# Kernel optimization log

Measured on AMD Instinct MI355X. Metric: run time of the kernel, lower is better.

## Reference

```python
import jax, jax.numpy as jnp
import numpy as np

V, D, NL, B, S = 32000, 512, 6, 2, 2048
H, N, K, DI = 8, 16, 4, 1024  # num_heads, d_state, d_conv, d_inner
TOT = DI + DI + H + H * N + H * N  # 2312


def setup_inputs() -> dict:
    key = jax.random.key(0)
    ks = jax.random.split(key, 12)
    tokens = jax.random.randint(ks[0], (B, S), 0, V, dtype=jnp.int32)
    embed = jax.random.normal(ks[1], (V, D), jnp.float32) * 0.02
    rms_w = jnp.ones((NL, D), jnp.float32)
    in_proj_w = jax.random.normal(ks[2], (NL, TOT, D), jnp.float32) * 0.02
    conv_w = jax.random.normal(ks[3], (NL, DI, K), jnp.float32) * 0.2
    dt_bias = jax.random.normal(ks[4], (NL, H), jnp.float32)
    A_log = jnp.tile(jnp.log(0.001 + jnp.arange(1, H + 1, dtype=jnp.float32)), (NL, 1))
    y_proj_w = jax.random.normal(ks[5], (NL, DI, H), jnp.float32) * 0.1
    out_proj_w = jax.random.normal(ks[6], (NL, D, DI), jnp.float32) * 0.02
    ln_w = jnp.ones((D,), jnp.float32)
    ln_b = jnp.zeros((D,), jnp.float32)
    head_w = jax.random.normal(ks[7], (V, D), jnp.float32) * 0.02
    head_b = jnp.zeros((V,), jnp.float32)
    return dict(tokens=tokens, embed=embed, rms_w=rms_w, in_proj_w=in_proj_w,
                conv_w=conv_w, dt_bias=dt_bias, A_log=A_log, y_proj_w=y_proj_w,
                out_proj_w=out_proj_w, ln_w=ln_w, ln_b=ln_b, head_w=head_w, head_b=head_b)


def _mamba_block(x, rms_w, W_in, cw, dtb, alog, yw, ow):
    res = x
    # RMSNorm
    xn = x * jax.lax.rsqrt(jnp.mean(x * x, -1, keepdims=True) + 1e-6) * rms_w
    p = jnp.einsum('bsd,td->bst', xn, W_in)  # [B,S,TOT]
    z = p[..., :DI]
    xi = p[..., DI:2 * DI]
    dt = p[..., 2 * DI:2 * DI + H]
    Bm = p[..., 2 * DI + H:2 * DI + H + H * N].reshape(B, S, H, N)
    Cm = p[..., 2 * DI + H + H * N:].reshape(B, S, H, N)
    # causal depthwise conv (pad left K-1, slice to S)
    xp = jnp.pad(xi, ((0, 0), (K - 1, 0), (0, 0)))
    xi = sum(xp[:, k:k + S, :] * cw[:, k] for k in range(K))
    xi = jax.nn.silu(xi)
    dt = jax.nn.softplus(dt + dtb)            # [B,S,H]
    A = -jnp.exp(alog)                        # [H]
    dA = jnp.exp(dt[..., None] * A[None, None, :, None])  # [B,S,H,N]
    xh = xi.reshape(B, S, H, DI // H)
    x_in = xh.mean(-1, keepdims=True)         # [B,S,H,1]
    u = dt[..., None] * x_in * Bm             # [B,S,H,N]

    def step(h, t):
        dA_t, u_t, C_t = t
        h = dA_t * h + u_t
        return h, (h * C_t).sum(-1)

    h0 = jnp.zeros((B, H, N), x.dtype)
    _, y = jax.lax.scan(step, h0, (dA.transpose(1, 0, 2, 3),
                                   u.transpose(1, 0, 2, 3),
                                   Cm.transpose(1, 0, 2, 3)))
    y = y.transpose(1, 0, 2)                  # [B,S,H]
    y = jnp.einsum('bsh,ih->bsi', y, yw)      # ad-hoc H->d_inner projection
    y = y * jax.nn.silu(z)
    return jnp.einsum('bsi,di->bsd', y, ow) + res


def reference(tokens, embed, rms_w, in_proj_w, conv_w, dt_bias, A_log,
              y_proj_w, out_proj_w, ln_w, ln_b, head_w, head_b):
    x = embed[tokens]                          # [B,S,D]
    for i in range(NL):
        x = _mamba_block(x, rms_w[i], in_proj_w[i], conv_w[i], dt_bias[i],
                         A_log[i], y_proj_w[i], out_proj_w[i])
    mu = x.mean(-1, keepdims=True)
    var = ((x - mu) ** 2).mean(-1, keepdims=True)
    x = (x - mu) * jax.lax.rsqrt(var + 1e-5) * ln_w + ln_b
    return jnp.einsum('bsd,vd->bsv', x, head_w) + head_b
```

## Files before the change

### kernel.cpp

```cpp
#include <hip/hip_runtime.h>
#include <math.h>

#define VV 32000
#define DD 512
#define NLAYER 6
#define BB 2
#define SS 2048
#define HH 8
#define NST 16
#define KC 4
#define DI 1024
#define TOT 2312
#define TOTP 2432
#define BS (BB*SS)
#define CHUNK 32
#define NCHUNK (SS/CHUNK)

typedef __attribute__((ext_vector_type(8))) short short8;
typedef __attribute__((ext_vector_type(4))) float f32x4;

__device__ __forceinline__ unsigned short f2bf(float f) {
    unsigned u = __float_as_uint(f);
    u += 0x7fff + ((u >> 16) & 1);
    return (unsigned short)(u >> 16);
}
__device__ __forceinline__ float bf2f(unsigned short h) {
    return __uint_as_float(((unsigned)h) << 16);
}

__device__ __forceinline__ void gload_lds16(const void* g, void* l) {
    __builtin_amdgcn_global_load_lds((const __attribute__((address_space(1))) void*)g,
                                     (__attribute__((address_space(3))) void*)l,
                                     16, 0, 0);
}

__global__ void split_kernel(const float* __restrict__ src,
                             unsigned short* __restrict__ hi,
                             unsigned short* __restrict__ lo,
                             int n_real, int n_pad) {
    int idx = (blockIdx.x * blockDim.x + threadIdx.x) * 4;
    if (idx >= n_pad) return;
    float4 v = make_float4(0.f, 0.f, 0.f, 0.f);
    if (idx < n_real) v = *(const float4*)(src + idx);
    float a[4] = {v.x, v.y, v.z, v.w};
    ushort4 hv, lv;
    unsigned short* hp = (unsigned short*)&hv;
    unsigned short* lp = (unsigned short*)&lv;
    #pragma unroll
    for (int j = 0; j < 4; ++j) {
        unsigned short h = f2bf(a[j]);
        hp[j] = h;
        lp[j] = f2bf(a[j] - bf2f(h));
    }
    *(ushort4*)(hi + idx) = hv;
    *(ushort4*)(lo + idx) = lv;
}

__global__ void embed_kernel(const int* __restrict__ tokens,
                             const float* __restrict__ embed,
                             float* __restrict__ x) {
    int row = blockIdx.x;
    int tok = tokens[row];
    const float4* src = (const float4*)(embed + (size_t)tok * DD);
    float4* dst = (float4*)(x + (size_t)row * DD);
    dst[threadIdx.x] = src[threadIdx.x];
}

__global__ void rmsnorm_kernel(const float* __restrict__ x,
                               const float* __restrict__ w,
                               unsigned short* __restrict__ xh,
                               unsigned short* __restrict__ xl) {
    int row = blockIdx.x;
    int tid = threadIdx.x;
    const float* xr = x + (size_t)row * DD;
    float a = xr[tid], b = xr[tid + 256];
    float v = a * a + b * b;
    for (int off = 32; off > 0; off >>= 1) v += __shfl_down(v, off, 64);
    __shared__ float wsum[4];
    if ((tid & 63) == 0) wsum[tid >> 6] = v;
    __syncthreads();
    float tot = wsum[0] + wsum[1] + wsum[2] + wsum[3];
    float sc = rsqrtf(tot * (1.0f / DD) + 1e-6f);
    float o0 = a * sc * w[tid];
    float o1 = b * sc * w[tid + 256];
    size_t base = (size_t)row * DD;
    unsigned short h0 = f2bf(o0), h1 = f2bf(o1);
    xh[base + tid]       = h0; xl[base + tid]       = f2bf(o0 - bf2f(h0));
    xh[base + tid + 256] = h1; xl[base + tid + 256] = f2bf(o1 - bf2f(h1));
}

template <int ADD_SRC, int ADD_BIAS>
__global__ __launch_bounds__(256) void gemm_mfma(
        const unsigned short* __restrict__ Ah, const unsigned short* __restrict__ Al,
        const unsigned short* __restrict__ Bh, const unsigned short* __restrict__ Bl,
        const float* __restrict__ src, const float* __restrict__ bias,
        float* __restrict__ C, int N, int Kd)
{
    __shared__ __align__(16) unsigned short As[128 * 32];
    __shared__ __align__(16) unsigned short Bs[128 * 32];
    const int tid  = threadIdx.x;
    const int lane = tid & 63;
    const int w    = tid >> 6;
    const int wr   = w >> 1, wc = w & 1;
    const int m0 = blockIdx.y * 128;
    const int n0 = blockIdx.x * 128;

    f32x4 acc[4][4] = {};

    int s0v = tid, s1v = 256 + tid;
    int row0 = s0v >> 2, row1 = s1v >> 2;
    int q0 = (s0v & 3) ^ (row0 & 3);
    int q1 = (s1v & 3) ^ (row1 & 3);
    char* ldsA0 = (char*)As + (w * 64) * 16;
    char* ldsA1 = (char*)As + (256 + w * 64) * 16;
    char* ldsB0 = (char*)Bs + (w * 64) * 16;
    char* ldsB1 = (char*)Bs + (256 + w * 64) * 16;

    const char* ra[4]; const char* rb[4];
    #pragma unroll
    for (int i = 0; i < 4; ++i) {
        int rrow = wr * 64 + i * 16 + (lane & 15);
        ra[i] = (const char*)As + rrow * 64 + (((lane >> 4) ^ (rrow & 3)) * 16);
        int crow = wc * 64 + i * 16 + (lane & 15);
        rb[i] = (const char*)Bs + crow * 64 + (((lane >> 4) ^ (crow & 3)) * 16);
    }

    #pragma unroll 1
    for (int ph = 0; ph < 3; ++ph) {
        const unsigned short* pA = (ph == 1) ? Al : Ah;
        const unsigned short* pB = (ph == 2) ? Bl : Bh;
        const unsigned short* gA0 = pA + (size_t)(m0 + row0) * Kd + q0 * 8;
        const unsigned short* gA1 = pA + (size_t)(m0 + row1) * Kd + q1 * 8;
        const unsigned short* gB0 = pB + (size_t)(n0 + row0) * Kd + q0 * 8;
        const unsigned short* gB1 = pB + (size_t)(n0 + row1) * Kd + q1 * 8;
        for (int k0 = 0; k0 < Kd; k0 += 32) {
            gload_lds16(gA0 + k0, ldsA0);
            gload_lds16(gA1 + k0, ldsA1);
            gload_lds16(gB0 + k0, ldsB0);
            gload_lds16(gB1 + k0, ldsB1);
            __syncthreads();
            short8 af[4], bf[4];
            #pragma unroll
            for (int i = 0; i < 4; ++i) af[i] = *(const short8*)ra[i];
            #pragma unroll
            for (int j = 0; j < 4; ++j) bf[j] = *(const short8*)rb[j];
            #pragma unroll
            for (int i = 0; i < 4; ++i)
                #pragma unroll
                for (int j = 0; j < 4; ++j)
                    acc[i][j] = __builtin_amdgcn_mfma_f32_16x16x32_bf16(af[i], bf[j], acc[i][j], 0, 0, 0);
            __syncthreads();
        }
    }

    #pragma unroll
    for (int i = 0; i < 4; ++i) {
        int rbase = m0 + wr * 64 + i * 16 + (lane >> 4) * 4;
        #pragma unroll
        for (int j = 0; j < 4; ++j) {
            int col = n0 + wc * 64 + j * 16 + (lane & 15);
            if (col < N) {
                #pragma unroll
                for (int p2 = 0; p2 < 4; ++p2) {
                    size_t o = (size_t)(rbase + p2) * N + col;
                    float vv = acc[i][j][p2];
                    if (ADD_SRC) vv += src[o];
                    if (ADD_BIAS) vv += bias[col];
                    C[o] = vv;
                }
            }
        }
    }
}

__global__ void conv_state_kernel(const float* __restrict__ p,
                                  const float* __restrict__ cw,
                                  const float* __restrict__ dtb,
                                  const float* __restrict__ alog,
                                  float* __restrict__ x_in,
                                  float* __restrict__ dtv,
                                  float* __restrict__ dAv) {
    int bs = blockIdx.x;
    int s = bs & (SS - 1);
    int tid = threadIdx.x;
    const float* prow = p + (size_t)bs * TOT + DI;
    float hacc = 0.f;
    #pragma unroll
    for (int j = 0; j < 4; ++j) {
        int c = tid * 4 + j;
        const float* w = cw + c * KC;
        float v = w[3] * prow[c];
        if (s >= 1) v += w[2] * prow[c - TOT];
        if (s >= 2) v += w[1] * prow[c - 2 * TOT];
        if (s >= 3) v += w[0] * prow[c - 3 * TOT];
        float sv = v / (1.f + expf(-v));
        hacc += sv;
    }
    for (int off = 16; off > 0; off >>= 1) hacc += __shfl_down(hacc, off, 32);
    __shared__ float hs[HH];
    if ((tid & 31) == 0) hs[tid >> 5] = hacc;
    __syncthreads();
    if (tid < HH) {
        x_in[(size_t)bs * HH + tid] = hs[tid] * (1.f / 128.f);
        float raw = p[(size_t)bs * TOT + 2 * DI + tid] + dtb[tid];
        float dt = (raw > 20.f) ? raw : log1pf(expf(raw));
        float A = -expf(alog[tid]);
        dtv[(size_t)bs * HH + tid] = dt;
        dAv[(size_t)bs * HH + tid] = expf(dt * A);
    }
}

__global__ void scan_phaseA(const float* __restrict__ p,
                            const float* __restrict__ x_in,
                            const float* __restrict__ dtv,
                            const float* __restrict__ dAv,
                            float* __restrict__ carryP,
                            float* __restrict__ hend) {
    int wid = blockIdx.x;
    int cg = wid & (NCHUNK / 4 - 1);
    int bh = wid / (NCHUNK / 4);
    int b = bh >> 3, h = bh & 7;
    int lane = threadIdx.x;
    int csub = lane >> 4, n = lane & 15;
    int chunk = cg * 4 + csub;
    int s0 = chunk * CHUNK;
    float hn = 0.f, P = 1.f;
    const float* pB = p + 2 * DI + HH + h * NST + n;
    for (int t = 0; t < CHUNK; ++t) {
        int idx = b * SS + s0 + t;
        float da = dAv[(size_t)idx * HH + h];
        float u = dtv[(size_t)idx * HH + h] * x_in[(size_t)idx * HH + h] * pB[(size_t)idx * TOT];
        hn = fmaf(da, hn, u);
        P *= da;
    }
    hend[((size_t)bh * NCHUNK + chunk) * NST + n] = hn;
    if (n == 0) carryP[(size_t)bh * NCHUNK + chunk] = P;
}

__global__ void scan_phaseB(const float* __restrict__ carryP,
                            const float* __restrict__ hend,
                            float* __restrict__ hstart) {
    int t = threadIdx.x;
    int bh = t >> 4, n = t & 15;
    float hc = 0.f;
    for (int c = 0; c < NCHUNK; ++c) {
        size_t base = (size_t)bh * NCHUNK + c;
        hstart[base * NST + n] = hc;
        hc = carryP[base] * hc + hend[base * NST + n];
    }
}

__global__ void scan_phaseC(const float* __restrict__ p,
                            const float* __restrict__ x_in,
                            const float* __restrict__ dtv,
                            const float* __restrict__ dAv,
                            const float* __restrict__ hstart,
                            float* __restrict__ y) {
    int wid = blockIdx.x;
    int cg = wid & (NCHUNK / 4 - 1);
    int bh = wid / (NCHUNK / 4);
    int b = bh >> 3, h = bh & 7;
    int lane = threadIdx.x;
    int csub = lane >> 4, n = lane & 15;
    int chunk = cg * 4 + csub;
    int s0 = chunk * CHUNK;
    float hn = hstart[((size_t)bh * NCHUNK + chunk) * NST + n];
    const float* pB = p + 2 * DI + HH + h * NST + n;
    const float* pC = pB + HH * NST;
    for (int t = 0; t < CHUNK; ++t) {
        int idx = b * SS + s0 + t;
        float da = dAv[(size_t)idx * HH + h];
        float u = dtv[(size_t)idx * HH + h] * x_in[(size_t)idx * HH + h] * pB[(size_t)idx * TOT];
        hn = fmaf(da, hn, u);
        float contrib = hn * pC[(size_t)idx * TOT];
        for (int off = 8; off > 0; off >>= 1) contrib += __shfl_down(contrib, off, 16);
        if (n == 0) y[(size_t)idx * HH + h] = contrib;
    }
}

__global__ void gate_kernel(const float* __restrict__ p,
                            const float* __restrict__ y,
                            const float* __restrict__ yw,
                            unsigned short* __restrict__ gh,
                            unsigned short* __restrict__ gl) {
    int bs = blockIdx.x;
    int tid = threadIdx.x;
    __shared__ float ys[HH];
    if (tid < HH) ys[tid] = y[(size_t)bs * HH + tid];
    __syncthreads();
    const float* prow = p + (size_t)bs * TOT;
    float outv[4];
    #pragma unroll
    for (int j = 0; j < 4; ++j) {
        int i = tid * 4 + j;
        const float* wv = yw + i * HH;
        float yd = 0.f;
        #pragma unroll
        for (int h = 0; h < HH; ++h) yd = fmaf(ys[h], wv[h], yd);
        float z = prow[i];
        float sz = z / (1.f + expf(-z));
        outv[j] = yd * sz;
    }
    ushort4 hv, lv;
    unsigned short* hp = (unsigned short*)&hv;
    unsigned short* lp = (unsigned short*)&lv;
    #pragma unroll
    for (int j = 0; j < 4; ++j) {
        unsigned short h = f2bf(outv[j]);
        hp[j] = h;
        lp[j] = f2bf(outv[j] - bf2f(h));
    }
    *(ushort4*)(gh + (size_t)bs * DI + tid * 4) = hv;
    *(ushort4*)(gl + (size_t)bs * DI + tid * 4) = lv;
}

__global__ void layernorm_kernel(const float* __restrict__ x,
                                 const float* __restrict__ w,
                                 const float* __restrict__ bbias,
                                 unsigned short* __restrict__ oh,
                                 unsigned short* __restrict__ ol) {
    int row = blockIdx.x;
    int tid = threadIdx.x;
    const float* xr = x + (size_t)row * DD;
    float a = xr[tid], c = xr[tid + 256];
    float sum = a + c;
    for (int off = 32; off > 0; off >>= 1) sum += __shfl_down(sum, off, 64);
    __shared__ float w1[4];
    __shared__ float w2[4];
    if ((tid & 63) == 0) w1[tid >> 6] = sum;
    __syncthreads();
    float mu = (w1[0] + w1[1] + w1[2] + w1[3]) * (1.0f / DD);
    float da = a - mu, dc = c - mu;
    float v = da * da + dc * dc;
    for (int off = 32; off > 0; off >>= 1) v += __shfl_down(v, off, 64);
    if ((tid & 63) == 0) w2[tid >> 6] = v;
    __syncthreads();
    float var = (w2[0] + w2[1] + w2[2] + w2[3]) * (1.0f / DD);
    float sc = rsqrtf(var + 1e-5f);
    float o0 = da * sc * w[tid] + bbias[tid];
    float o1 = dc * sc * w[tid + 256] + bbias[tid + 256];
    size_t base = (size_t)row * DD;
    unsigned short h0 = f2bf(o0), h1 = f2bf(o1);
    oh[base + tid]       = h0; ol[base + tid]       = f2bf(o0 - bf2f(h0));
    oh[base + tid + 256] = h1; ol[base + tid + 256] = f2bf(o1 - bf2f(h1));
}

extern "C" void kernel_launch(void* const* d_in, const int* in_sizes, int n_in,
                              void* d_out, int out_size, void* d_ws, size_t ws_size,
                              hipStream_t stream) {
    const int*   tokens   = (const int*)d_in[0];
    const float* embed    = (const float*)d_in[1];
    const float* rms_w    = (const float*)d_in[2];
    const float* in_proj  = (const float*)d_in[3];
    const float* conv_w   = (const float*)d_in[4];
    const float* dt_bias  = (const float*)d_in[5];
    const float* A_log    = (const float*)d_in[6];
    const float* y_proj   = (const float*)d_in[7];
    const float* out_proj = (const float*)d_in[8];
    const float* ln_w     = (const float*)d_in[9];
    const float* ln_b     = (const float*)d_in[10];
    const float* head_w   = (const float*)d_in[11];
    const float* head_b   = (const float*)d_in[12];
    float* out = (float*)d_out;

    float* ws = (float*)d_ws;
    size_t off = 0;
    float* x      = ws + off; off += (size_t)BS * DD;
    float* p      = ws + off; off += (size_t)BS * TOT;
    float* x_in   = ws + off; off += (size_t)BS * HH;
    float* dtv    = ws + off; off += (size_t)BS * HH;
    float* dAv    = ws + off; off += (size_t)BS * HH;
    float* y      = ws + off; off += (size_t)BS * HH;
    float* carryP = ws + off; off += (size_t)BB * HH * NCHUNK;
    float* hend   = ws + off; off += (size_t)BB * HH * NCHUNK * NST;
    float* hstart = ws + off; off += (size_t)BB * HH * NCHUNK * NST;
    unsigned short* xnh = (unsigned short*)(ws + off); off += (size_t)BS * DD / 2;
    unsigned short* xnl = (unsigned short*)(ws + off); off += (size_t)BS * DD / 2;
    unsigned short* gh  = (unsigned short*)(ws + off); off += (size_t)BS * DI / 2;
    unsigned short* gl  = (unsigned short*)(ws + off); off += (size_t)BS * DI / 2;
    unsigned short* wih = (unsigned short*)(ws + off); off += (size_t)NLAYER * TOTP * DD / 2;
    unsigned short* wil = (unsigned short*)(ws + off); off += (size_t)NLAYER * TOTP * DD / 2;
    unsigned short* woh = (unsigned short*)(ws + off); off += (size_t)NLAYER * DD * DI / 2;
    unsigned short* wol = (unsigned short*)(ws + off); off += (size_t)NLAYER * DD * DI / 2;
    unsigned short* whh = (unsigned short*)(ws + off); off += (size_t)VV * DD / 2;
    unsigned short* whl = (unsigned short*)(ws + off); off += (size_t)VV * DD / 2;

    for (int l = 0; l < NLAYER; ++l)
        split_kernel<<<TOTP * DD / 1024, 256, 0, stream>>>(
            in_proj + (size_t)l * TOT * DD,
            wih + (size_t)l * TOTP * DD, wil + (size_t)l * TOTP * DD,
            TOT * DD, TOTP * DD);
    split_kernel<<<NLAYER * DD * DI / 1024, 256, 0, stream>>>(
            out_proj, woh, wol, NLAYER * DD * DI, NLAYER * DD * DI);
    split_kernel<<<VV * DD / 1024, 256, 0, stream>>>(
            head_w, whh, whl, VV * DD, VV * DD);

    embed_kernel<<<BS, 128, 0, stream>>>(tokens, embed, x);

    for (int l = 0; l < NLAYER; ++l) {
        rmsnorm_kernel<<<BS, 256, 0, stream>>>(x, rms_w + l * DD, xnh, xnl);

        dim3 g1(TOTP / 128, BS / 128);
        gemm_mfma<0, 0><<<g1, 256, 0, stream>>>(xnh, xnl,
            wih + (size_t)l * TOTP * DD, wil + (size_t)l * TOTP * DD,
            nullptr, nullptr, p, TOT, DD);

        conv_state_kernel<<<BS, 256, 0, stream>>>(p, conv_w + l * DI * KC,
                                                  dt_bias + l * HH, A_log + l * HH,
                                                  x_in, dtv, dAv);

        scan_phaseA<<<BB * HH * (NCHUNK / 4), 64, 0, stream>>>(p, x_in, dtv, dAv, carryP, hend);
        scan_phaseB<<<1, 256, 0, stream>>>(carryP, hend, hstart);
        scan_phaseC<<<BB * HH * (NCHUNK / 4), 64, 0, stream>>>(p, x_in, dtv, dAv, hstart, y);

        gate_kernel<<<BS, 256, 0, stream>>>(p, y, y_proj + (size_t)l * DI * HH, gh, gl);

        dim3 g2(DD / 128, BS / 128);
        gemm_mfma<1, 0><<<g2, 256, 0, stream>>>(gh, gl,
            woh + (size_t)l * DD * DI, wol + (size_t)l * DD * DI,
            x, nullptr, x, DD, DI);
    }

    layernorm_kernel<<<BS, 256, 0, stream>>>(x, ln_w, ln_b, xnh, xnl);

    dim3 g3(VV / 128, BS / 128);
    gemm_mfma<0, 1><<<g3, 256, 0, stream>>>(xnh, xnl, whh, whl,
        nullptr, head_b, out, VV, DD);
}
```

Baseline: 2.374 ms.

## Fuse split-bf16 GEMM phases into one K loop, add XCD-aware tile mapping

```diff
diff --git a/kernel.cpp b/kernel.cpp
--- a/kernel.cpp
+++ b/kernel.cpp
@@ -89,76 +89,127 @@
     xh[base + tid + 256] = h1; xl[base + tid + 256] = f2bf(o1 - bf2f(h1));
 }
 
-template <int ADD_SRC, int ADD_BIAS>
+template <int BM, int BN, int ADD_SRC, int ADD_BIAS>
 __global__ __launch_bounds__(256) void gemm_mfma(
         const unsigned short* __restrict__ Ah, const unsigned short* __restrict__ Al,
         const unsigned short* __restrict__ Bh, const unsigned short* __restrict__ Bl,
         const float* __restrict__ src, const float* __restrict__ bias,
-        float* __restrict__ C, int N, int Kd)
+        float* __restrict__ C, int M, int N, int Kd)
 {
-    __shared__ __align__(16) unsigned short As[128 * 32];
-    __shared__ __align__(16) unsigned short Bs[128 * 32];
+    constexpr int WM = BM / 2, WN = BN / 2;
+    constexpr int MI = WM / 16, NJ = WN / 16;
+    constexpr int ASLOTS = BM * 4;
+    constexpr int BSLOTS = BN * 4;
+    constexpr int RA = ASLOTS / 256;
+    constexpr int RB = BSLOTS / 256;
+    constexpr int OFF_AH = 0;
+    constexpr int OFF_AL = ASLOTS * 16;
+    constexpr int OFF_BH = 2 * ASLOTS * 16;
+    constexpr int OFF_BL = OFF_BH + BSLOTS * 16;
+
+    __shared__ __align__(16) char lds[(2 * ASLOTS + 2 * BSLOTS) * 16];
+
     const int tid  = threadIdx.x;
     const int lane = tid & 63;
     const int w    = tid >> 6;
     const int wr   = w >> 1, wc = w & 1;
-    const int m0 = blockIdx.y * 128;
-    const int n0 = blockIdx.x * 128;
-
-    f32x4 acc[4][4] = {};
-
-    int s0v = tid, s1v = 256 + tid;
-    int row0 = s0v >> 2, row1 = s1v >> 2;
-    int q0 = (s0v & 3) ^ (row0 & 3);
-    int q1 = (s1v & 3) ^ (row1 & 3);
-    char* ldsA0 = (char*)As + (w * 64) * 16;
-    char* ldsA1 = (char*)As + (256 + w * 64) * 16;
-    char* ldsB0 = (char*)Bs + (w * 64) * 16;
-    char* ldsB1 = (char*)Bs + (256 + w * 64) * 16;
-
-    const char* ra[4]; const char* rb[4];
-    #pragma unroll
-    for (int i = 0; i < 4; ++i) {
-        int rrow = wr * 64 + i * 16 + (lane & 15);
-        ra[i] = (const char*)As + rrow * 64 + (((lane >> 4) ^ (rrow & 3)) * 16);
-        int crow = wc * 64 + i * 16 + (lane & 15);
-        rb[i] = (const char*)Bs + crow * 64 + (((lane >> 4) ^ (crow & 3)) * 16);
-    }
-
-    #pragma unroll 1
-    for (int ph = 0; ph < 3; ++ph) {
-        const unsigned short* pA = (ph == 1) ? Al : Ah;
-        const unsigned short* pB = (ph == 2) ? Bl : Bh;
-        const unsigned short* gA0 = pA + (size_t)(m0 + row0) * Kd + q0 * 8;
-        const unsigned short* gA1 = pA + (size_t)(m0 + row1) * Kd + q1 * 8;
-        const unsigned short* gB0 = pB + (size_t)(n0 + row0) * Kd + q0 * 8;
-        const unsigned short* gB1 = pB + (size_t)(n0 + row1) * Kd + q1 * 8;
-        for (int k0 = 0; k0 < Kd; k0 += 32) {
-            gload_lds16(gA0 + k0, ldsA0);
-            gload_lds16(gA1 + k0, ldsA1);
-            gload_lds16(gB0 + k0, ldsB0);
-            gload_lds16(gB1 + k0, ldsB1);
-            __syncthreads();
-            short8 af[4], bf[4];
+
+    int bid = blockIdx.x;
+    int nwg = gridDim.x;
+    int xcd = bid & 7, lid = bid >> 3;
+    int q8 = nwg >> 3, r8 = nwg & 7;
+    int wg = (xcd < r8 ? xcd * (q8 + 1) : r8 * (q8 + 1) + (xcd - r8) * q8) + lid;
+    int nmb = M / BM;
+    int m0 = (wg % nmb) * BM;
+    int n0 = (wg / nmb) * BN;
+
+    f32x4 acc[MI][NJ] = {};
+
+    const unsigned short *gAh[RA], *gAl[RA];
+    const unsigned short *gBh[RB], *gBl[RB];
+    char *dAh[RA], *dAl[RA], *dBh[RB], *dBl[RB];
+    #pragma unroll
+    for (int rd = 0; rd < RA; ++rd) {
+        int s = rd * 256 + tid;
+        int row = s >> 2;
+        int qs = (s & 3) ^ ((row ^ (row >> 2)) & 3);
+        size_t go = (size_t)(m0 + row) * Kd + qs * 8;
+        gAh[rd] = Ah + go; gAl[rd] = Al + go;
+        int dslot = (rd * 256 + w * 64) * 16;
+        dAh[rd] = lds + OFF_AH + dslot;
+        dAl[rd] = lds + OFF_AL + dslot;
+    }
+    #pragma unroll
+    for (int rd = 0; rd < RB; ++rd) {
+        int s = rd * 256 + tid;
+        int row = s >> 2;
+        int qs = (s & 3) ^ ((row ^ (row >> 2)) & 3);
+        size_t go = (size_t)(n0 + row) * Kd + qs * 8;
+        gBh[rd] = Bh + go; gBl[rd] = Bl + go;
+        int dslot = (rd * 256 + w * 64) * 16;
+        dBh[rd] = lds + OFF_BH + dslot;
+        dBl[rd] = lds + OFF_BL + dslot;
+    }
+
+    const char *rah[MI], *ral[MI], *rbh[NJ], *rbl[NJ];
+    #pragma unroll
+    for (int i = 0; i < MI; ++i) {
+        int row = wr * WM + i * 16 + (lane & 15);
+        int q = (lane >> 4) ^ ((row ^ (row >> 2)) & 3);
+        int o = row * 64 + q * 16;
+        rah[i] = lds + OFF_AH + o;
+        ral[i] = lds + OFF_AL + o;
+    }
+    #pragma unroll
+    for (int j = 0; j < NJ; ++j) {
+        int row = wc * WN + j * 16 + (lane & 15);
+        int q = (lane >> 4) ^ ((row ^ (row >> 2)) & 3);
+        int o = row * 64 + q * 16;
+        rbh[j] = lds + OFF_BH + o;
+        rbl[j] = lds + OFF_BL + o;
+    }
+
+    for (int k0 = 0; k0 < Kd; k0 += 32) {
+        #pragma unroll
+        for (int rd = 0; rd < RA; ++rd) {
+            gload_lds16(gAh[rd] + k0, dAh[rd]);
+            gload_lds16(gAl[rd] + k0, dAl[rd]);
+        }
+        #pragma unroll
+        for (int rd = 0; rd < RB; ++rd) {
+            gload_lds16(gBh[rd] + k0, dBh[rd]);
+            gload_lds16(gBl[rd] + k0, dBl[rd]);
+        }
+        __syncthreads();
+        short8 ah[MI], al[MI], bh[NJ], bl[NJ];
+        #pragma unroll
+        for (int i = 0; i < MI; ++i) { ah[i] = *(const short8*)rah[i]; al[i] = *(const short8*)ral[i]; }
+        #pragma unroll
+        for (int j = 0; j < NJ; ++j) { bh[j] = *(const short8*)rbh[j]; bl[j] = *(const short8*)rbl[j]; }
+        #pragma unroll
+        for (int i = 0; i < MI; ++i)
             #pragma unroll
-            for (int i = 0; i < 4; ++i) af[i] = *(const short8*)ra[i];
+            for (int j = 0; j < NJ; ++j)
+                acc[i][j] = __builtin_amdgcn_mfma_f32_16x16x32_bf16(ah[i], bh[j], acc[i][j], 0, 0, 0);
+        #pragma unroll
+        for (int i = 0; i < MI; ++i)
             #pragma unroll
-            for (int j = 0; j < 4; ++j) bf[j] = *(const short8*)rb[j];
+            for (int j = 0; j < NJ; ++j)
+                acc[i][j] = __builtin_amdgcn_mfma_f32_16x16x32_bf16(al[i], bh[j], acc[i][j], 0, 0, 0);
+        #pragma unroll
+        for (int i = 0; i < MI; ++i)
             #pragma unroll
-            for (int i = 0; i < 4; ++i)
-                #pragma unroll
-                for (int j = 0; j < 4; ++j)
-                    acc[i][j] = __builtin_amdgcn_mfma_f32_16x16x32_bf16(af[i], bf[j], acc[i][j], 0, 0, 0);
-            __syncthreads();
-        }
-    }
-
-    #pragma unroll
-    for (int i = 0; i < 4; ++i) {
-        int rbase = m0 + wr * 64 + i * 16 + (lane >> 4) * 4;
-        #pragma unroll
-        for (int j = 0; j < 4; ++j) {
-            int col = n0 + wc * 64 + j * 16 + (lane & 15);
+            for (int j = 0; j < NJ; ++j)
+                acc[i][j] = __builtin_amdgcn_mfma_f32_16x16x32_bf16(ah[i], bl[j], acc[i][j], 0, 0, 0);
+        __syncthreads();
+    }
+
+    #pragma unroll
+    for (int i = 0; i < MI; ++i) {
+        int rbase = m0 + wr * WM + i * 16 + (lane >> 4) * 4;
+        #pragma unroll
+        for (int j = 0; j < NJ; ++j) {
+            int col = n0 + wc * WN + j * 16 + (lane & 15);
             if (col < N) {
                 #pragma unroll
                 for (int p2 = 0; p2 < 4; ++p2) {
@@ -400,10 +451,10 @@
     for (int l = 0; l < NLAYER; ++l) {
         rmsnorm_kernel<<<BS, 256, 0, stream>>>(x, rms_w + l * DD, xnh, xnl);
 
-        dim3 g1(TOTP / 128, BS / 128);
-        gemm_mfma<0, 0><<<g1, 256, 0, stream>>>(xnh, xnl,
+        gemm_mfma<128, 128, 0, 0><<<(BS / 128) * (TOTP / 128), 256, 0, stream>>>(
+            xnh, xnl,
             wih + (size_t)l * TOTP * DD, wil + (size_t)l * TOTP * DD,
-            nullptr, nullptr, p, TOT, DD);
+            nullptr, nullptr, p, BS, TOT, DD);
 
         conv_state_kernel<<<BS, 256, 0, stream>>>(p, conv_w + l * DI * KC,
                                                   dt_bias + l * HH, A_log + l * HH,
@@ -415,15 +466,15 @@
 
         gate_kernel<<<BS, 256, 0, stream>>>(p, y, y_proj + (size_t)l * DI * HH, gh, gl);
 
-        dim3 g2(DD / 128, BS / 128);
-        gemm_mfma<1, 0><<<g2, 256, 0, stream>>>(gh, gl,
+        gemm_mfma<64, 64, 1, 0><<<(BS / 64) * (DD / 64), 256, 0, stream>>>(
+            gh, gl,
             woh + (size_t)l * DD * DI, wol + (size_t)l * DD * DI,
-            x, nullptr, x, DD, DI);
+            x, nullptr, x, BS, DD, DI);
     }
 
     layernorm_kernel<<<BS, 256, 0, stream>>>(x, ln_w, ln_b, xnh, xnl);
 
-    dim3 g3(VV / 128, BS / 128);
-    gemm_mfma<0, 1><<<g3, 256, 0, stream>>>(xnh, xnl, whh, whl,
-        nullptr, head_b, out, VV, DD);
-}
+    gemm_mfma<128, 128, 0, 1><<<(BS / 128) * (VV / 128), 256, 0, stream>>>(
+        xnh, xnl, whh, whl,
+        nullptr, head_b, out, BS, VV, DD);
+}
```

New measurement: 2.024 ms. -14.8%, faster.
